# Optimization experiments

Hardware: AMD Instinct MI355X
Metric: run time of the kernel (lower is better)

Reference implementation:

```python
import jax, jax.numpy as jnp
import numpy as np

N = 131072
IN_A = 256
IN_V = 512
IN_VF = 512
CH = 256
BN_EPS = 1e-5
COS_EPS = 1e-8


def setup_inputs() -> dict:
    key = jax.random.key(0)
    ks = jax.random.split(key, 12)
    s = 0.05
    return {
        "x": jax.random.normal(ks[0], (N, 4, 512), dtype=jnp.float32),
        "audio_node_mask": jax.random.bernoulli(ks[1], 0.5, (N,)),
        "W_a": jax.random.normal(ks[2], (IN_A, CH), dtype=jnp.float32) * s,
        "b_a": jnp.zeros((CH,), jnp.float32),
        "W_v": jax.random.normal(ks[3], (IN_V, CH), dtype=jnp.float32) * s,
        "b_v": jnp.zeros((CH,), jnp.float32),
        "W_f": jax.random.normal(ks[4], (2 * CH, CH), dtype=jnp.float32) * s,
        "b_f": jnp.zeros((CH,), jnp.float32),
        "gamma": jnp.ones((CH,), jnp.float32),
        "beta": jnp.zeros((CH,), jnp.float32),
        "W_fc": jax.random.normal(ks[5], (CH, 2), dtype=jnp.float32) * s,
        "b_fc": jnp.zeros((2,), jnp.float32),
    }


def reference(x, audio_node_mask, W_a, b_a, W_v, b_v, W_f, b_f, gamma, beta, W_fc, b_fc):
    # Slice per-type features (x: [N, 4, 512])
    a_in = x[:, 0, :IN_A]    # audio feats (also video->audio feats)
    v_in = x[:, 1, :IN_V]    # video feats
    a_vf = x[:, 2, :IN_VF]   # audio voice-face emb
    v_vf = x[:, 3, :IN_VF]   # video voice-face emb

    # cosine similarity along feature dim (torch.nn.functional.cosine_similarity semantics)
    dot = jnp.sum(a_vf * v_vf, axis=1)
    denom = jnp.maximum(jnp.linalg.norm(a_vf, axis=1) * jnp.linalg.norm(v_vf, axis=1), COS_EPS)
    sim = dot / denom  # [N]

    # per-type linears (compute densely, select by mask -> same math as masked scatter)
    a_out = a_in @ W_a + b_a                                   # [N, CH]
    v_out = v_in @ W_v + b_v                                   # [N, CH]
    va = a_in * sim[:, None]                                   # sim-weighted audio feats on video nodes
    fused = jnp.concatenate([va, v_out], axis=1) @ W_f + b_f   # [N, CH]

    graph_feats = jnp.where(audio_node_mask[:, None], a_out, fused)

    # BatchNorm1d (training: batch statistics, biased variance)
    mu = jnp.mean(graph_feats, axis=0)
    var = jnp.mean(jnp.square(graph_feats - mu), axis=0)
    graph_feats = (graph_feats - mu) * jax.lax.rsqrt(var + BN_EPS) * gamma + beta

    graph_feats = jax.nn.relu(graph_feats)
    return graph_feats @ W_fc + b_fc  # [N, 2]
```

## Files before the change

### kernel.cpp

```cpp
#include <hip/hip_runtime.h>
#include <hip/hip_bf16.h>
#include <stdint.h>

#define NN 131072

typedef unsigned int uint;
typedef unsigned short ushort;
typedef __attribute__((ext_vector_type(8))) __bf16 bf16x8;
typedef __attribute__((ext_vector_type(2))) __bf16 bf16x2;
typedef __attribute__((ext_vector_type(4))) float f32x4;


__device__ __forceinline__ ushort f2bf(float f) {
    uint u = __float_as_uint(f);
    u += 0x7FFF + ((u >> 16) & 1);
    return (ushort)(u >> 16);
}
__device__ __forceinline__ uint pk2(float a, float b) {
    bf16x2 t;
    t[0] = (__bf16)a;
    t[1] = (__bf16)b;
    return __builtin_bit_cast(uint, t);
}
__device__ __forceinline__ bool mask_val(const unsigned char* m8, int flag, int i) {
    return flag ? (m8[(size_t)i * 4] != 0) : (m8[i] != 0);
}
__device__ __forceinline__ size_t pack_off(int k, int c) {
    return (size_t)(((k >> 5) * 16 + (c >> 4)) * 512
                    + (((k >> 3) & 3) * 16 + (c & 15)) * 8 + (k & 7));
}

__global__ void k_detect(const uint* m32, int n, int* flag) {
    __shared__ int cnt;
    if (threadIdx.x == 0) cnt = 0;
    __syncthreads();
    int local = 0;
    int nw = n >> 2;
    for (int i = threadIdx.x; i < nw; i += 1024)
        if (m32[i] & 0x0000FF00u) local = 1;
    if (local) atomicAdd(&cnt, 1);
    __syncthreads();
    if (threadIdx.x == 0) *flag = (cnt == 0) ? 1 : 0;
}

__global__ void k_count(const unsigned char* m8, const int* flagp, int* cntM) {
    int flag = *flagp;
    int t = threadIdx.x;
    bool m = mask_val(m8, flag, blockIdx.x * 256 + t);
    unsigned long long bal = __ballot(m);
    __shared__ int wsum[4];
    if ((t & 63) == 0) wsum[t >> 6] = __popcll(bal);
    __syncthreads();
    if (t == 0) cntM[blockIdx.x] = wsum[0] + wsum[1] + wsum[2] + wsum[3];
}

__global__ void k_scan(const int* __restrict__ cntM, int* __restrict__ meta,
                       int* __restrict__ baseA, int* __restrict__ baseF) {
    __shared__ int sA[512], sF[512];
    int t = threadIdx.x;
    int a = cntM[t], f = 256 - a;
    sA[t] = a; sF[t] = f;
    __syncthreads();
    for (int off = 1; off < 512; off <<= 1) {
        int va = (t >= off) ? sA[t - off] : 0;
        int vf = (t >= off) ? sF[t - off] : 0;
        __syncthreads();
        sA[t] += va; sF[t] += vf;
        __syncthreads();
    }
    baseA[t] = sA[t] - a;
    baseF[t] = sF[t] - f;
    if (t == 511) { meta[2] = sA[511]; meta[1] = sF[511]; }
}

__global__ void k_fill(const unsigned char* m8, const int* flagp,
                       const int* __restrict__ baseA, const int* __restrict__ baseF,
                       int* __restrict__ audioIdx, int* __restrict__ fusedIdx) {
    int flag = *flagp;
    int blk = blockIdx.x, t = threadIdx.x;
    int row = blk * 256 + t;
    bool m = mask_val(m8, flag, row);
    unsigned long long bal = __ballot(m);
    int lane = t & 63, w = t >> 6;
    unsigned long long lt = (1ull << lane) - 1ull;
    int pA = __popcll(bal & lt);
    __shared__ int wA[4];
    if (lane == 0) wA[w] = __popcll(bal);
    __syncthreads();
    int offA = 0;
    for (int i = 0; i < w; ++i) offA += wA[i];
    int offF = w * 64 - offA;
    int pF = lane - pA;
    if (m) audioIdx[baseA[blk] + offA + pA] = row;
    else   fusedIdx[baseF[blk] + offF + pF] = row;
}

__global__ void k_prep(const float* __restrict__ Wa, const float* __restrict__ Wf,
                       const float* __restrict__ Wv, const float* __restrict__ bv,
                       const float* __restrict__ bf_, ushort* __restrict__ Bwa,
                       ushort* __restrict__ Bwf, float* __restrict__ cf) {
    int c = threadIdx.x;
    int b = blockIdx.x;
    if (b < 256) {
        Bwa[pack_off(b, c)] = f2bf(Wa[b * 256 + c]);
    } else if (b < 512) {
        Bwf[pack_off(512 + (b - 256), c)] = f2bf(Wf[(b - 256) * 256 + c]);
    } else if (b < 1024) {
        int k = b - 512;
        const float* wr = Wv + k * 256;
        float acc = 0.f;
        for (int j = 0; j < 256; ++j) acc += wr[j] * Wf[(256 + j) * 256 + c];
        Bwf[pack_off(k, c)] = f2bf(acc);
    } else {
        float acc = bf_[c];
        for (int j = 0; j < 256; ++j) acc += bv[j] * Wf[(256 + j) * 256 + c];
        cf[c] = acc;
    }
}

__global__ __launch_bounds__(512, 4) void k_main(
    const float* __restrict__ x, const int* __restrict__ meta,
    const int* __restrict__ fusedIdx, const int* __restrict__ audioIdx,
    const ushort* __restrict__ Bwa, const ushort* __restrict__ Bwf,
    const float* __restrict__ ba, const float* __restrict__ cf,
    ushort* __restrict__ gf, float* __restrict__ bn_s, float* __restrict__ bn_q)
{
    __shared__ bf16x8 As8[2][128 * 8];
    __shared__ int ridxS[128];
    __shared__ float simS[128];
    __shared__ unsigned char validS[128];
    __shared__ float redS[256], redQ[256];

    const int tid = threadIdx.x;
    const int cntF = meta[1], cntA = meta[2];
    const int nbF = (cntF + 127) >> 7;
    const int nbA = (cntA + 127) >> 7;
    const int b = blockIdx.x;
    const bool isF = b < nbF;
    const int bb = isF ? b : b - nbF;

    if (!isF && bb >= nbA) {
        if (tid < 256) {
            bn_s[(size_t)b * 256 + tid] = 0.f;
            bn_q[(size_t)b * 256 + tid] = 0.f;
        }
        return;
    }

    const int cnt = isF ? cntF : cntA;
    const int* idxArr = isF ? fusedIdx : audioIdx;
    const int lane = tid & 63;
    const int w = tid >> 6, wr = w >> 2, wc = w & 3;
    const int fr = lane & 15, fg = lane >> 4;

    if (tid < 128) {
        int gpos = bb * 128 + tid;
        int ok = gpos < cnt;
        ridxS[tid] = ok ? idxArr[gpos] : 0;
        validS[tid] = ok;
        simS[tid] = 1.f;
    }
    __syncthreads();

    const int NS = isF ? 12 : 4;
    const int sr = tid >> 2, sk = tid & 3;
    const float* xrow = x + (size_t)ridxS[sr] * 2048;
    const float sVf = validS[sr] ? 1.f : 0.f;
    float sAf = 0.f;

    int4 pA_A[2], pA_B[2];
    auto loadA = [&](int st, int4* p) {
        const float scl = (isF && st >= 8) ? sAf : sVf;
        const int off = isF ? ((st < 8) ? 512 + st * 64 : (st - 8) * 64) : st * 64;
        const float4* src = (const float4*)(xrow + off + sk * 16);
        #pragma unroll
        for (int s = 0; s < 2; ++s) {
            float4 u0 = src[2 * s], u1 = src[2 * s + 1];
            int4 q;
            q.x = pk2(u0.x * scl, u0.y * scl);
            q.y = pk2(u0.z * scl, u0.w * scl);
            q.z = pk2(u1.x * scl, u1.y * scl);
            q.w = pk2(u1.z * scl, u1.w * scl);
            p[s] = q;
        }
    };
    auto storeA = [&](int buf, const int4* p) {
        #pragma unroll
        for (int s = 0; s < 2; ++s)
            As8[buf][sr * 8 + ((sk * 2 + s) ^ (sr & 7))] = __builtin_bit_cast(bf16x8, p[s]);
    };

    const ushort* bBase = (isF ? Bwf : Bwa) + ((size_t)(wc * 4) << 9) + (lane << 3);

    f32x4 acc[4][4];
    #pragma unroll
    for (int m = 0; m < 4; ++m)
        #pragma unroll
        for (int n = 0; n < 4; ++n) acc[m][n] = (f32x4){0.f, 0.f, 0.f, 0.f};

    auto compute = [&](int buf, int st) {
        #pragma unroll
        for (int kk = 0; kk < 2; ++kk) {
            bf16x8 af[4];
            #pragma unroll
            for (int m = 0; m < 4; ++m) {
                int r = wr * 64 + m * 16 + fr;
                af[m] = As8[buf][r * 8 + ((kk * 4 + fg) ^ (r & 7))];
            }
            #pragma unroll
            for (int n = 0; n < 4; ++n) {
                bf16x8 bv = *(const bf16x8*)(bBase + ((size_t)((st * 2 + kk) * 16 + n) << 9));
                #pragma unroll
                for (int m = 0; m < 4; ++m)
                    acc[m][n] = __builtin_amdgcn_mfma_f32_16x16x32_bf16(
                        af[m], bv, acc[m][n], 0, 0, 0);
            }
        }
    };

    loadA(0, pA_A);

    if (isF) {
        #pragma unroll 2
        for (int rr = 0; rr < 16; ++rr) {
            int r = w * 16 + rr;
            const float4* p = (const float4*)(x + (size_t)ridxS[r] * 2048 + 1024);
            float4 a0 = p[lane], a1 = p[lane + 64];
            float4 v0 = p[lane + 128], v1 = p[lane + 192];
            float dot = a0.x * v0.x + a0.y * v0.y + a0.z * v0.z + a0.w * v0.w
                      + a1.x * v1.x + a1.y * v1.y + a1.z * v1.z + a1.w * v1.w;
            float na = a0.x * a0.x + a0.y * a0.y + a0.z * a0.z + a0.w * a0.w
                     + a1.x * a1.x + a1.y * a1.y + a1.z * a1.z + a1.w * a1.w;
            float nv = v0.x * v0.x + v0.y * v0.y + v0.z * v0.z + v0.w * v0.w
                     + v1.x * v1.x + v1.y * v1.y + v1.z * v1.z + v1.w * v1.w;
            #pragma unroll
            for (int off = 32; off; off >>= 1) {
                dot += __shfl_xor(dot, off);
                na  += __shfl_xor(na,  off);
                nv  += __shfl_xor(nv,  off);
            }
            if (lane == 0)
                simS[r] = dot / fmaxf(sqrtf(na) * sqrtf(nv), 1e-8f);
        }
    }
    __syncthreads();
    sAf = validS[sr] ? simS[sr] : 0.f;

    storeA(0, pA_A);
    loadA(1, pA_B);
    __syncthreads();

    for (int st = 0; st < NS; st += 2) {
        if (st + 2 < NS) loadA(st + 2, pA_A);
        compute(0, st);
        storeA(1, pA_B);
        __syncthreads();
        if (st + 3 < NS) loadA(st + 3, pA_B);
        compute(1, st + 1);
        if (st + 2 < NS) storeA(0, pA_A);
        __syncthreads();
    }

    if (tid < 256) { redS[tid] = 0.f; redQ[tid] = 0.f; }
    __syncthreads();

    const int colLo = wc * 64 + fr;
    const float* biasp = isF ? cf : ba;
    float bN[4];
    #pragma unroll
    for (int n = 0; n < 4; ++n) bN[n] = biasp[colLo + n * 16];

    float cs[4] = {0.f, 0.f, 0.f, 0.f}, cq[4] = {0.f, 0.f, 0.f, 0.f};
    #pragma unroll
    for (int m = 0; m < 4; ++m) {
        #pragma unroll
        for (int j = 0; j < 4; ++j) {
            int rloc = wr * 64 + m * 16 + fg * 4 + j;
            if (!validS[rloc]) continue;
            ushort* grow = gf + (size_t)ridxS[rloc] * 256;
            #pragma unroll
            for (int n = 0; n < 4; ++n) {
                float g = acc[m][n][j] + bN[n];
                grow[colLo + n * 16] = f2bf(g);
                cs[n] += g;
                cq[n] += g * g;
            }
        }
    }
    #pragma unroll
    for (int n = 0; n < 4; ++n) {
        atomicAdd(&redS[colLo + n * 16], cs[n]);
        atomicAdd(&redQ[colLo + n * 16], cq[n]);
    }
    __syncthreads();
    if (tid < 256) {
        bn_s[(size_t)b * 256 + tid] = redS[tid];
        bn_q[(size_t)b * 256 + tid] = redQ[tid];
    }
}

__global__ void k_stats(const float* __restrict__ bn_s, const float* __restrict__ bn_q,
                        const float* __restrict__ gamma, const float* __restrict__ beta,
                        float* __restrict__ scale, float* __restrict__ shift) {
    int c = blockIdx.x;
    int t = threadIdx.x;
    float s = 0.f, q = 0.f;
    for (int r = t; r < 1025; r += 256) {
        s += bn_s[(size_t)r * 256 + c];
        q += bn_q[(size_t)r * 256 + c];
    }
    __shared__ float ss[256], qq[256];
    ss[t] = s; qq[t] = q;
    __syncthreads();
    for (int off = 128; off; off >>= 1) {
        if (t < off) { ss[t] += ss[t + off]; qq[t] += qq[t + off]; }
        __syncthreads();
    }
    if (t == 0) {
        float mu  = ss[0] / 131072.f;
        float var = qq[0] / 131072.f - mu * mu;
        float sc = gamma[c] * rsqrtf(var + 1e-5f);
        scale[c] = sc;
        shift[c] = beta[c] - mu * sc;
    }
}

__global__ void k_out(const ushort* __restrict__ gf, const float* __restrict__ scale,
                      const float* __restrict__ shift, const float* __restrict__ Wfc,
                      const float* __restrict__ bfc, float* __restrict__ out) {
    int wid = threadIdx.x >> 6;
    int lane = threadIdx.x & 63;
    int i = blockIdx.x * 4 + wid;
    uint2 gv = ((const uint2*)(gf + (size_t)i * 256))[lane];
    float g0 = __uint_as_float(gv.x << 16);
    float g1 = __uint_as_float(gv.x & 0xFFFF0000u);
    float g2 = __uint_as_float(gv.y << 16);
    float g3 = __uint_as_float(gv.y & 0xFFFF0000u);
    int c0 = lane * 4;
    float4 sc = *(const float4*)(scale + c0);
    float4 sh = *(const float4*)(shift + c0);
    float y0 = fmaxf(g0 * sc.x + sh.x, 0.f);
    float y1 = fmaxf(g1 * sc.y + sh.y, 0.f);
    float y2 = fmaxf(g2 * sc.z + sh.z, 0.f);
    float y3 = fmaxf(g3 * sc.w + sh.w, 0.f);
    const float4* w = (const float4*)(Wfc + c0 * 2);
    float4 w0 = w[0], w1 = w[1];
    float p0 = y0 * w0.x + y1 * w0.z + y2 * w1.x + y3 * w1.z;
    float p1 = y0 * w0.y + y1 * w0.w + y2 * w1.y + y3 * w1.w;
    #pragma unroll
    for (int off = 32; off; off >>= 1) {
        p0 += __shfl_xor(p0, off);
        p1 += __shfl_xor(p1, off);
    }
    if (lane == 0) {
        out[(size_t)i * 2]     = p0 + bfc[0];
        out[(size_t)i * 2 + 1] = p1 + bfc[1];
    }
}

extern "C" void kernel_launch(void* const* d_in, const int* in_sizes, int n_in,
                              void* d_out, int out_size, void* d_ws, size_t ws_size,
                              hipStream_t stream) {
    const float* x          = (const float*)d_in[0];
    const unsigned char* mk = (const unsigned char*)d_in[1];
    const float* Wa  = (const float*)d_in[2];
    const float* ba  = (const float*)d_in[3];
    const float* Wv  = (const float*)d_in[4];
    const float* bv  = (const float*)d_in[5];
    const float* Wf  = (const float*)d_in[6];
    const float* bf  = (const float*)d_in[7];
    const float* gamma = (const float*)d_in[8];
    const float* beta  = (const float*)d_in[9];
    const float* Wfc = (const float*)d_in[10];
    const float* bfc = (const float*)d_in[11];
    float* out = (float*)d_out;

    char* ws = (char*)d_ws;
    int*    meta   = (int*)ws;
    float*  scale  = (float*)(ws + 1024);
    float*  shift  = (float*)(ws + 2048);
    float*  cf     = (float*)(ws + 3072);
    int*    cntM   = (int*)(ws + 8192);
    int*    baseA  = (int*)(ws + 12288);
    int*    baseF  = (int*)(ws + 16384);
    ushort* Bwa    = (ushort*)(ws + 32768);
    ushort* Bwf    = (ushort*)(ws + 262144);
    int*    fusedIdx = (int*)(ws + (1u << 20));
    int*    audioIdx = (int*)(ws + (1u << 20) + (512u << 10));
    float*  bn_s   = (float*)(ws + (2u << 20));
    float*  bn_q   = (float*)(ws + (4u << 20));
    ushort* gf     = (ushort*)(ws + (8u << 20));

    int n = in_sizes[1];

    k_detect<<<1, 1024, 0, stream>>>((const uint*)mk, n, meta);
    k_count<<<512, 256, 0, stream>>>(mk, meta, cntM);
    k_scan<<<1, 512, 0, stream>>>(cntM, meta, baseA, baseF);
    k_fill<<<512, 256, 0, stream>>>(mk, meta, baseA, baseF, audioIdx, fusedIdx);
    k_prep<<<1025, 256, 0, stream>>>(Wa, Wf, Wv, bv, bf, Bwa, Bwf, cf);
    k_main<<<1025, 512, 0, stream>>>(x, meta, fusedIdx, audioIdx, Bwa, Bwf, ba, cf,
                                     gf, bn_s, bn_q);
    k_stats<<<256, 256, 0, stream>>>(bn_s, bn_q, gamma, beta, scale, shift);
    k_out<<<NN / 4, 256, 0, stream>>>(gf, scale, shift, Wfc, bfc, out);
}
```

Measured before the change: 245.1 us.

## Parallelize mask format detection, simplify main pipeline, widen output loads

The single-block mask-format detection kernel becomes a 128-block kernel that writes per-block nonzero flags. The count and fill kernels then combine those flags in shared memory, which removes a serial scan over the mask. The main GEMM loop drops its two-register double-buffer unroll for a simpler one-stage prefetch loop, which may cut register pressure but exposes more load latency. The output kernel now handles two rows per wavefront with 16-byte loads, and the weight-prep dot-product loops are unrolled.

```diff
diff --git a/kernel.cpp b/kernel.cpp
--- a/kernel.cpp
+++ b/kernel.cpp
@@ -3,6 +3,7 @@
 #include <stdint.h>
 
 #define NN 131072
+#define NB_MAIN 1025
 
 typedef unsigned int uint;
 typedef unsigned short ushort;
@@ -30,22 +31,29 @@
                     + (((k >> 3) & 3) * 16 + (c & 15)) * 8 + (k & 7));
 }
 
-__global__ void k_detect(const uint* m32, int n, int* flag) {
-    __shared__ int cnt;
-    if (threadIdx.x == 0) cnt = 0;
-    __syncthreads();
-    int local = 0;
-    int nw = n >> 2;
-    for (int i = threadIdx.x; i < nw; i += 1024)
-        if (m32[i] & 0x0000FF00u) local = 1;
-    if (local) atomicAdd(&cnt, 1);
-    __syncthreads();
-    if (threadIdx.x == 0) *flag = (cnt == 0) ? 1 : 0;
-}
-
-__global__ void k_count(const unsigned char* m8, const int* flagp, int* cntM) {
-    int flag = *flagp;
+__global__ void k_nz(const uint* m32, int* nzArr) {
     int t = threadIdx.x;
+    uint v = m32[blockIdx.x * 256 + t];
+    unsigned long long bal = __ballot((v & 0x0000FF00u) != 0);
+    __shared__ int s[4];
+    if ((t & 63) == 0) s[t >> 6] = (bal != 0) ? 1 : 0;
+    __syncthreads();
+    if (t == 0) nzArr[blockIdx.x] = s[0] | s[1] | s[2] | s[3];
+}
+
+__device__ __forceinline__ int get_flag(const int* nzArr, int t) {
+    __shared__ int nzsh;
+    if (t == 0) nzsh = 0;
+    __syncthreads();
+    if (t < 128 && nzArr[t]) nzsh = 1;
+    __syncthreads();
+    return nzsh ? 0 : 1;
+}
+
+__global__ void k_count(const unsigned char* m8, const int* __restrict__ nzArr,
+                        int* cntM) {
+    int t = threadIdx.x;
+    int flag = get_flag(nzArr, t);
     bool m = mask_val(m8, flag, blockIdx.x * 256 + t);
     unsigned long long bal = __ballot(m);
     __shared__ int wsum[4];
@@ -73,11 +81,11 @@
     if (t == 511) { meta[2] = sA[511]; meta[1] = sF[511]; }
 }
 
-__global__ void k_fill(const unsigned char* m8, const int* flagp,
+__global__ void k_fill(const unsigned char* m8, const int* __restrict__ nzArr,
                        const int* __restrict__ baseA, const int* __restrict__ baseF,
                        int* __restrict__ audioIdx, int* __restrict__ fusedIdx) {
-    int flag = *flagp;
     int blk = blockIdx.x, t = threadIdx.x;
+    int flag = get_flag(nzArr, t);
     int row = blk * 256 + t;
     bool m = mask_val(m8, flag, row);
     unsigned long long bal = __ballot(m);
@@ -109,10 +117,12 @@
         int k = b - 512;
         const float* wr = Wv + k * 256;
         float acc = 0.f;
+        #pragma unroll 8
         for (int j = 0; j < 256; ++j) acc += wr[j] * Wf[(256 + j) * 256 + c];
         Bwf[pack_off(k, c)] = f2bf(acc);
     } else {
         float acc = bf_[c];
+        #pragma unroll 8
         for (int j = 0; j < 256; ++j) acc += bv[j] * Wf[(256 + j) * 256 + c];
         cf[c] = acc;
     }
@@ -168,8 +178,8 @@
     const float sVf = validS[sr] ? 1.f : 0.f;
     float sAf = 0.f;
 
-    int4 pA_A[2], pA_B[2];
-    auto loadA = [&](int st, int4* p) {
+    int4 pA[2];
+    auto loadA = [&](int st) {
         const float scl = (isF && st >= 8) ? sAf : sVf;
         const int off = isF ? ((st < 8) ? 512 + st * 64 : (st - 8) * 64) : st * 64;
         const float4* src = (const float4*)(xrow + off + sk * 16);
@@ -181,13 +191,13 @@
             q.y = pk2(u0.z * scl, u0.w * scl);
             q.z = pk2(u1.x * scl, u1.y * scl);
             q.w = pk2(u1.z * scl, u1.w * scl);
-            p[s] = q;
+            pA[s] = q;
         }
     };
-    auto storeA = [&](int buf, const int4* p) {
+    auto storeA = [&](int buf) {
         #pragma unroll
         for (int s = 0; s < 2; ++s)
-            As8[buf][sr * 8 + ((sk * 2 + s) ^ (sr & 7))] = __builtin_bit_cast(bf16x8, p[s]);
+            As8[buf][sr * 8 + ((sk * 2 + s) ^ (sr & 7))] = __builtin_bit_cast(bf16x8, pA[s]);
     };
 
     const ushort* bBase = (isF ? Bwf : Bwa) + ((size_t)(wc * 4) << 9) + (lane << 3);
@@ -218,7 +228,7 @@
         }
     };
 
-    loadA(0, pA_A);
+    loadA(0);
 
     if (isF) {
         #pragma unroll 2
@@ -246,18 +256,13 @@
     __syncthreads();
     sAf = validS[sr] ? simS[sr] : 0.f;
 
-    storeA(0, pA_A);
-    loadA(1, pA_B);
-    __syncthreads();
-
-    for (int st = 0; st < NS; st += 2) {
-        if (st + 2 < NS) loadA(st + 2, pA_A);
-        compute(0, st);
-        storeA(1, pA_B);
-        __syncthreads();
-        if (st + 3 < NS) loadA(st + 3, pA_B);
-        compute(1, st + 1);
-        if (st + 2 < NS) storeA(0, pA_A);
+    storeA(0);
+    __syncthreads();
+
+    for (int st = 0; st < NS; ++st) {
+        if (st + 1 < NS) loadA(st + 1);
+        compute(st & 1, st);
+        if (st + 1 < NS) storeA((st + 1) & 1);
         __syncthreads();
     }
 
@@ -305,7 +310,7 @@
     int c = blockIdx.x;
     int t = threadIdx.x;
     float s = 0.f, q = 0.f;
-    for (int r = t; r < 1025; r += 256) {
+    for (int r = t; r < NB_MAIN; r += 256) {
         s += bn_s[(size_t)r * 256 + c];
         q += bn_q[(size_t)r * 256 + c];
     }
@@ -330,29 +335,35 @@
                       const float* __restrict__ bfc, float* __restrict__ out) {
     int wid = threadIdx.x >> 6;
     int lane = threadIdx.x & 63;
-    int i = blockIdx.x * 4 + wid;
-    uint2 gv = ((const uint2*)(gf + (size_t)i * 256))[lane];
-    float g0 = __uint_as_float(gv.x << 16);
-    float g1 = __uint_as_float(gv.x & 0xFFFF0000u);
-    float g2 = __uint_as_float(gv.y << 16);
-    float g3 = __uint_as_float(gv.y & 0xFFFF0000u);
-    int c0 = lane * 4;
-    float4 sc = *(const float4*)(scale + c0);
-    float4 sh = *(const float4*)(shift + c0);
-    float y0 = fmaxf(g0 * sc.x + sh.x, 0.f);
-    float y1 = fmaxf(g1 * sc.y + sh.y, 0.f);
-    float y2 = fmaxf(g2 * sc.z + sh.z, 0.f);
-    float y3 = fmaxf(g3 * sc.w + sh.w, 0.f);
-    const float4* w = (const float4*)(Wfc + c0 * 2);
-    float4 w0 = w[0], w1 = w[1];
-    float p0 = y0 * w0.x + y1 * w0.z + y2 * w1.x + y3 * w1.z;
-    float p1 = y0 * w0.y + y1 * w0.w + y2 * w1.y + y3 * w1.w;
-    #pragma unroll
-    for (int off = 32; off; off >>= 1) {
+    int hl = lane & 31;
+    int i = blockIdx.x * 8 + wid * 2 + (lane >> 5);
+    uint4 gv = ((const uint4*)(gf + (size_t)i * 256))[hl];
+    int c0 = hl * 8;
+    float g[8];
+    g[0] = __uint_as_float(gv.x << 16); g[1] = __uint_as_float(gv.x & 0xFFFF0000u);
+    g[2] = __uint_as_float(gv.y << 16); g[3] = __uint_as_float(gv.y & 0xFFFF0000u);
+    g[4] = __uint_as_float(gv.z << 16); g[5] = __uint_as_float(gv.z & 0xFFFF0000u);
+    g[6] = __uint_as_float(gv.w << 16); g[7] = __uint_as_float(gv.w & 0xFFFF0000u);
+    float p0 = 0.f, p1 = 0.f;
+    #pragma unroll
+    for (int j = 0; j < 2; ++j) {
+        f32x4 sc = *(const f32x4*)(scale + c0 + j * 4);
+        f32x4 sh = *(const f32x4*)(shift + c0 + j * 4);
+        f32x4 w0 = *(const f32x4*)(Wfc + (c0 + j * 4) * 2);
+        f32x4 w1 = *(const f32x4*)(Wfc + (c0 + j * 4) * 2 + 4);
+        float y0 = fmaxf(g[j * 4 + 0] * sc.x + sh.x, 0.f);
+        float y1 = fmaxf(g[j * 4 + 1] * sc.y + sh.y, 0.f);
+        float y2 = fmaxf(g[j * 4 + 2] * sc.z + sh.z, 0.f);
+        float y3 = fmaxf(g[j * 4 + 3] * sc.w + sh.w, 0.f);
+        p0 += y0 * w0.x + y1 * w0.z + y2 * w1.x + y3 * w1.z;
+        p1 += y0 * w0.y + y1 * w0.w + y2 * w1.y + y3 * w1.w;
+    }
+    #pragma unroll
+    for (int off = 16; off; off >>= 1) {
         p0 += __shfl_xor(p0, off);
         p1 += __shfl_xor(p1, off);
     }
-    if (lane == 0) {
+    if (hl == 0) {
         out[(size_t)i * 2]     = p0 + bfc[0];
         out[(size_t)i * 2 + 1] = p1 + bfc[1];
     }
@@ -383,6 +394,7 @@
     int*    cntM   = (int*)(ws + 8192);
     int*    baseA  = (int*)(ws + 12288);
     int*    baseF  = (int*)(ws + 16384);
+    int*    nzArr  = (int*)(ws + 20480);
     ushort* Bwa    = (ushort*)(ws + 32768);
     ushort* Bwf    = (ushort*)(ws + 262144);
     int*    fusedIdx = (int*)(ws + (1u << 20));
@@ -391,15 +403,13 @@
     float*  bn_q   = (float*)(ws + (4u << 20));
     ushort* gf     = (ushort*)(ws + (8u << 20));
 
-    int n = in_sizes[1];
-
-    k_detect<<<1, 1024, 0, stream>>>((const uint*)mk, n, meta);
-    k_count<<<512, 256, 0, stream>>>(mk, meta, cntM);
+    k_nz<<<128, 256, 0, stream>>>((const uint*)mk, nzArr);
+    k_count<<<512, 256, 0, stream>>>(mk, nzArr, cntM);
     k_scan<<<1, 512, 0, stream>>>(cntM, meta, baseA, baseF);
-    k_fill<<<512, 256, 0, stream>>>(mk, meta, baseA, baseF, audioIdx, fusedIdx);
+    k_fill<<<512, 256, 0, stream>>>(mk, nzArr, baseA, baseF, audioIdx, fusedIdx);
     k_prep<<<1025, 256, 0, stream>>>(Wa, Wf, Wv, bv, bf, Bwa, Bwf, cf);
-    k_main<<<1025, 512, 0, stream>>>(x, meta, fusedIdx, audioIdx, Bwa, Bwf, ba, cf,
-                                     gf, bn_s, bn_q);
+    k_main<<<NB_MAIN, 512, 0, stream>>>(x, meta, fusedIdx, audioIdx, Bwa, Bwf, ba, cf,
+                                        gf, bn_s, bn_q);
     k_stats<<<256, 256, 0, stream>>>(bn_s, bn_q, gamma, beta, scale, shift);
-    k_out<<<NN / 4, 256, 0, stream>>>(gf, scale, shift, Wfc, bfc, out);
-}
+    k_out<<<NN / 8, 256, 0, stream>>>(gf, scale, shift, Wfc, bfc, out);
+}
```

Measured after the change: 255.9 us. 1.04x slower.
